# Performance work log

Measured on AMD Instinct MI355X. Metric: run time of the kernel, lower is better.

The kernel has to match this reference:

```python
import jax, jax.numpy as jnp
import numpy as np

N, E = 20000, 100000
D_IN, H1, C1 = 512, 8, 64   # conv1: 512 -> 8 heads x 64, concat -> 512
H2, C2 = 4, 128             # conv2: 512 -> 4 heads x 128, mean -> 128


def setup_inputs() -> dict:
    key = jax.random.key(0)
    k = jax.random.split(key, 12)
    s_in = 1.0 / np.sqrt(D_IN).astype(np.float32)
    return {
        "street_embedding": jax.random.normal(k[0], (N, D_IN), jnp.float32),
        "edge_index": jax.random.randint(k[1], (2, E), 0, N),
        "y": jax.random.randint(k[2], (N,), 0, C2),
        "train_mask": jax.random.bernoulli(k[3], 0.5, (N,)),
        "W1": jax.random.normal(k[4], (D_IN, H1 * C1), jnp.float32) * s_in,
        "att_src1": jax.random.normal(k[5], (H1, C1), jnp.float32) * 0.1,
        "att_dst1": jax.random.normal(k[6], (H1, C1), jnp.float32) * 0.1,
        "b1": jnp.zeros((H1 * C1,), jnp.float32),
        "W2": jax.random.normal(k[7], (H1 * C1, H2 * C2), jnp.float32) * s_in,
        "att_src2": jax.random.normal(k[8], (H2, C2), jnp.float32) * 0.1,
        "att_dst2": jax.random.normal(k[9], (H2, C2), jnp.float32) * 0.1,
        "b2": jnp.zeros((C2,), jnp.float32),
    }


def _gat_conv(x, W, a_src, a_dst, b, src, dst, n, H, C, concat):
    # linear transform (no bias, as in PyG GATConv's internal lin)
    xp = (x @ W).reshape(n, H, C)                      # [N,H,C]
    asrc = jnp.einsum('nhc,hc->nh', xp, a_src)         # [N,H]
    adst = jnp.einsum('nhc,hc->nh', xp, a_dst)
    e = jax.nn.leaky_relu(asrc[src] + adst[dst], 0.2)  # [E',H] edge scores
    # softmax over incoming edges per destination node
    m = jax.lax.stop_gradient(jax.ops.segment_max(e, dst, num_segments=n))
    ex = jnp.exp(e - m[dst])
    denom = jax.ops.segment_sum(ex, dst, num_segments=n)
    alpha = ex / (denom[dst] + 1e-16)                  # [E',H]
    out = jax.ops.segment_sum(alpha[:, :, None] * xp[src], dst, num_segments=n)  # [N,H,C]
    if concat:
        return out.reshape(n, H * C) + b
    return out.mean(axis=1) + b


def reference(street_embedding, edge_index, y, train_mask,
              W1, att_src1, att_dst1, b1, W2, att_src2, att_dst2, b2):
    n = street_embedding.shape[0]
    loop = jnp.arange(n)
    # PyG GATConv adds self-loops by default
    src = jnp.concatenate([edge_index[0], loop])
    dst = jnp.concatenate([edge_index[1], loop])
    # dropout layers are identity in eval mode
    h = _gat_conv(street_embedding, W1, att_src1, att_dst1, b1, src, dst, n, H1, C1, True)
    h = jax.nn.elu(h)
    out = _gat_conv(h, W2, att_src2, att_dst2, b2, src, dst, n, H2, C2, False)  # [N,C2]
    # CrossEntropyLoss, mean over train_mask nodes (weighted mean, jit-safe)
    logp = jax.nn.log_softmax(out, axis=-1)
    ce = -jnp.take_along_axis(logp, y[:, None], axis=-1)[:, 0]
    w = train_mask.astype(out.dtype)
    loss_su = jnp.sum(w * ce) / jnp.sum(w)
    return (loss_su, out)
```

## Files before the change

### kernel.cpp

```cpp
#include <hip/hip_runtime.h>
#include <cmath>

#define D_IN 512
#define HC   512
#define NH1  8
#define NC1  64
#define NH2  4
#define NC2  128
#define BM 128
#define BN 128
#define BK 32

typedef __attribute__((ext_vector_type(8))) short short8;
typedef __attribute__((ext_vector_type(4))) float f32x4;

__device__ inline ushort f2bf(float f) {
  unsigned u = __float_as_uint(f);
  return (ushort)((u + 0x7FFFu + ((u >> 16) & 1u)) >> 16);
}
__device__ inline float bf2f(ushort b) { return __uint_as_float(((unsigned)b) << 16); }

__global__ void k_cast(const float* __restrict__ in, ushort* __restrict__ outp, int n4) {
  int i = blockIdx.x * blockDim.x + threadIdx.x;
  if (i >= n4) return;
  float4 v = ((const float4*)in)[i];
  ushort4 r = { f2bf(v.x), f2bf(v.y), f2bf(v.z), f2bf(v.w) };
  ((ushort4*)outp)[i] = r;
}

__global__ void k_castT(const float* __restrict__ W, ushort* __restrict__ Wt, int K, int N) {
  int idx = blockIdx.x * blockDim.x + threadIdx.x;
  if (idx >= K * N) return;
  int n = idx / K, k = idx - n * K;
  Wt[idx] = f2bf(W[(size_t)k * N + n]);
}

template<int H>
__global__ void k_gemm_bf16(const ushort* __restrict__ A, const ushort* __restrict__ Bt,
                            ushort* __restrict__ Cbf,
                            const float* __restrict__ att_s, const float* __restrict__ att_d,
                            float* __restrict__ asrc, float* __restrict__ adst, int M) {
  constexpr int C = HC / H;
  __shared__ __align__(16) ushort As[BM * BK];
  __shared__ __align__(16) ushort Bs[BN * BK];
  int t = threadIdx.x;
  int m0 = blockIdx.y * BM;
  int n0 = blockIdx.x * BN;
  int wave = t >> 6, lane = t & 63;
  int ln = lane & 15, qd = lane >> 4;
  int wm = (wave >> 1) * 64, wn = (wave & 1) * 64;

  f32x4 acc[4][4] = {};

  int g = t >> 6, ct = (t >> 4) & 3, lt = t & 15;
  int rA0 = m0 + g * 16 + lt;      if (rA0 > M - 1) rA0 = M - 1;
  int rA1 = m0 + 64 + g * 16 + lt; if (rA1 > M - 1) rA1 = M - 1;
  const ushort* gA0 = A + (size_t)rA0 * D_IN + ct * 8;
  const ushort* gA1 = A + (size_t)rA1 * D_IN + ct * 8;
  const ushort* gB0 = Bt + (size_t)(n0 + g * 16 + lt) * D_IN + ct * 8;
  const ushort* gB1 = Bt + (size_t)(n0 + 64 + g * 16 + lt) * D_IN + ct * 8;
  ushort* lA = As + t * 8;
  ushort* lB = Bs + t * 8;

  for (int k0 = 0; k0 < D_IN; k0 += BK) {
    __syncthreads();
    __builtin_amdgcn_global_load_lds((const __attribute__((address_space(1))) void*)(gA0 + k0),
                                     (__attribute__((address_space(3))) void*)lA, 16, 0, 0);
    __builtin_amdgcn_global_load_lds((const __attribute__((address_space(1))) void*)(gA1 + k0),
                                     (__attribute__((address_space(3))) void*)(lA + 2048), 16, 0, 0);
    __builtin_amdgcn_global_load_lds((const __attribute__((address_space(1))) void*)(gB0 + k0),
                                     (__attribute__((address_space(3))) void*)lB, 16, 0, 0);
    __builtin_amdgcn_global_load_lds((const __attribute__((address_space(1))) void*)(gB1 + k0),
                                     (__attribute__((address_space(3))) void*)(lB + 2048), 16, 0, 0);
    __syncthreads();
    short8 a[4], b[4];
#pragma unroll
    for (int i = 0; i < 4; ++i)
      a[i] = *(const short8*)&As[(((wave >> 1) * 4 + i) * 4 + qd) * 128 + ln * 8];
#pragma unroll
    for (int j = 0; j < 4; ++j)
      b[j] = *(const short8*)&Bs[(((wave & 1) * 4 + j) * 4 + qd) * 128 + ln * 8];
#pragma unroll
    for (int i = 0; i < 4; ++i)
#pragma unroll
      for (int j = 0; j < 4; ++j)
        acc[i][j] = __builtin_amdgcn_mfma_f32_16x16x32_bf16(a[i], b[j], acc[i][j], 0, 0, 0);
  }

#pragma unroll
  for (int i = 0; i < 4; ++i) {
#pragma unroll
    for (int reg = 0; reg < 4; ++reg) {
      int row = m0 + wm + i * 16 + qd * 4 + reg;
      if (row >= M) continue;
#pragma unroll
      for (int j = 0; j < 4; ++j)
        Cbf[(size_t)row * HC + n0 + wn + j * 16 + ln] = f2bf(acc[i][j][reg]);
    }
  }

  int colbase = n0 + wn;
  int h = colbase / C;
  float sa[4], da[4];
#pragma unroll
  for (int j = 0; j < 4; ++j) {
    int c = (colbase % C) + j * 16 + ln;
    sa[j] = att_s[h * C + c];
    da[j] = att_d[h * C + c];
  }
#pragma unroll
  for (int i = 0; i < 4; ++i) {
#pragma unroll
    for (int reg = 0; reg < 4; ++reg) {
      float ps = acc[i][0][reg] * sa[0] + acc[i][1][reg] * sa[1]
               + acc[i][2][reg] * sa[2] + acc[i][3][reg] * sa[3];
      float pd = acc[i][0][reg] * da[0] + acc[i][1][reg] * da[1]
               + acc[i][2][reg] * da[2] + acc[i][3][reg] * da[3];
#pragma unroll
      for (int o = 1; o < 16; o <<= 1) { ps += __shfl_xor(ps, o); pd += __shfl_xor(pd, o); }
      int row = m0 + wm + i * 16 + qd * 4 + reg;
      if (ln == 0 && row < M) {
        if (C == 64) { asrc[row * H + h] = ps; adst[row * H + h] = pd; }
        else { atomicAdd(&asrc[row * H + h], ps); atomicAdd(&adst[row * H + h], pd); }
      }
    }
  }
}

__global__ void k_hist(const int* __restrict__ ei, int E, int Etot, int* __restrict__ cnt) {
  int e = blockIdx.x * blockDim.x + threadIdx.x;
  if (e >= Etot) return;
  int d = (e < E) ? ei[E + e] : e - E;
  atomicAdd(&cnt[d], 1);
}

__global__ void k_scan(const int* __restrict__ cnt, int* __restrict__ rowstart, int N) {
  int tid = threadIdx.x;
  int T = (N + 1023) / 1024;
  int base = tid * T;
  int sum = 0;
  for (int i = 0; i < T; ++i) { int j = base + i; if (j < N) sum += cnt[j]; }
  int lane = tid & 63, w = tid >> 6;
  int v = sum;
#pragma unroll
  for (int off = 1; off < 64; off <<= 1) {
    int u = __shfl_up(v, off);
    if (lane >= off) v += u;
  }
  __shared__ int wsum[16];
  if (lane == 63) wsum[w] = v;
  __syncthreads();
  if (tid < 16) {
    int tv = wsum[tid];
#pragma unroll
    for (int off = 1; off < 16; off <<= 1) {
      int u = __shfl_up(tv, off);
      if (tid >= off) tv += u;
    }
    wsum[tid] = tv;
  }
  __syncthreads();
  int wave_prefix = (w == 0) ? 0 : wsum[w - 1];
  int run = wave_prefix + v - sum;
  for (int i = 0; i < T; ++i) {
    int j = base + i;
    if (j < N) { rowstart[j] = run; run += cnt[j]; }
  }
  if (tid == 1023) rowstart[N] = run;
}

__global__ void k_scatter(const int* __restrict__ ei, int E, int Etot,
                          const int* __restrict__ rowstart, int* __restrict__ cursor,
                          int* __restrict__ csr_src) {
  int e = blockIdx.x * blockDim.x + threadIdx.x;
  if (e >= Etot) return;
  int s = (e < E) ? ei[e] : e - E;
  int d = (e < E) ? ei[E + e] : e - E;
  int pos = atomicAdd(&cursor[d], 1);
  csr_src[rowstart[d] + pos] = s;
}

template<int H, int MODE>
__global__ void k_agg(const int* __restrict__ rowstart, const int* __restrict__ csr_src,
                      const float* __restrict__ asrc, const float* __restrict__ adst,
                      const ushort* __restrict__ xp, ushort* __restrict__ hout,
                      float* __restrict__ out2, const float* __restrict__ bias,
                      const int* __restrict__ y, const int* __restrict__ msk,
                      float* __restrict__ acc2, int N) {
  int n = blockIdx.x;
  int tid = threadIdx.x;
  constexpr int C = HC / H;
  int h = (tid * 4) / C;
  int beg = rowstart[n], end = rowstart[n + 1];

  __shared__ int   s_src[32];
  __shared__ float s_out[512];

  float adn = adst[n * H + h];
  float ax = 0.f, ay = 0.f, az = 0.f, aw = 0.f, wsum = 0.f;

  for (int c0 = beg; c0 < end; c0 += 32) {
    int len = end - c0; if (len > 32) len = 32;
    __syncthreads();
    if (tid < len) s_src[tid] = csr_src[c0 + tid];
    __syncthreads();
    for (int i = 0; i < len; ++i) {
      int s = s_src[i];
      float v = asrc[s * H + h] + adn;
      v = (v > 0.f) ? v : 0.2f * v;
      float w = __expf(v);
      ushort4 vv = ((const ushort4*)xp)[(size_t)s * 128 + tid];
      ax += w * bf2f(vv.x); ay += w * bf2f(vv.y);
      az += w * bf2f(vv.z); aw += w * bf2f(vv.w);
      wsum += w;
    }
  }
  float rdn = 1.0f / (wsum + 1e-16f);
  ax *= rdn; ay *= rdn; az *= rdn; aw *= rdn;

  if (MODE == 1) {
    int hc = tid * 4;
    float v0 = ax + bias[hc], v1 = ay + bias[hc + 1];
    float v2 = az + bias[hc + 2], v3 = aw + bias[hc + 3];
    v0 = (v0 > 0.f) ? v0 : expm1f(v0);
    v1 = (v1 > 0.f) ? v1 : expm1f(v1);
    v2 = (v2 > 0.f) ? v2 : expm1f(v2);
    v3 = (v3 > 0.f) ? v3 : expm1f(v3);
    ushort4 rr = { f2bf(v0), f2bf(v1), f2bf(v2), f2bf(v3) };
    ((ushort4*)hout)[(size_t)n * 128 + tid] = rr;
  } else {
    int hc = tid * 4;
    s_out[hc] = ax; s_out[hc + 1] = ay; s_out[hc + 2] = az; s_out[hc + 3] = aw;
    __syncthreads();
    if (tid < 32) {
#pragma unroll
      for (int k = 0; k < 4; ++k) {
        int c = tid * 4 + k;
        float sum = s_out[c] + s_out[128 + c] + s_out[256 + c] + s_out[384 + c];
        float lg = sum * 0.25f + bias[c];
        out2[(size_t)n * NC2 + c] = lg;
        s_out[c] = lg;
      }
    }
    __syncthreads();
    float lv = s_out[tid];
    int lane = tid & 63, wv = tid >> 6;
    float mx = lv;
#pragma unroll
    for (int o = 32; o > 0; o >>= 1) mx = fmaxf(mx, __shfl_xor(mx, o));
    if (lane == 0) s_out[256 + wv] = mx;
    __syncthreads();
    mx = fmaxf(s_out[256], s_out[257]);
    float e = __expf(lv - mx);
#pragma unroll
    for (int o = 32; o > 0; o >>= 1) e += __shfl_xor(e, o);
    if (lane == 0) s_out[260 + wv] = e;
    __syncthreads();
    if (tid == 0 && msk[n] != 0) {
      float se = s_out[260] + s_out[261];
      float ce = mx + logf(se) - s_out[y[n]];
      int slot = n & 127;
      atomicAdd(&acc2[slot], ce);
      atomicAdd(&acc2[128 + slot], 1.0f);
    }
  }
}

__global__ void k_final(const float* __restrict__ acc2, float* __restrict__ out0) {
  int tid = threadIdx.x;
  float ce = acc2[tid], ct = acc2[128 + tid];
#pragma unroll
  for (int o = 32; o > 0; o >>= 1) { ce += __shfl_xor(ce, o); ct += __shfl_xor(ct, o); }
  __shared__ float s[4];
  if ((tid & 63) == 0) { s[(tid >> 6) * 2] = ce; s[(tid >> 6) * 2 + 1] = ct; }
  __syncthreads();
  if (tid == 0) out0[0] = (s[0] + s[2]) / (s[1] + s[3]);
}

extern "C" void kernel_launch(void* const* d_in, const int* in_sizes, int n_in,
                              void* d_out, int out_size, void* d_ws, size_t ws_size,
                              hipStream_t stream) {
  const float* x   = (const float*)d_in[0];
  const int*   ei  = (const int*)d_in[1];
  const int*   y   = (const int*)d_in[2];
  const int*   msk = (const int*)d_in[3];
  const float* W1  = (const float*)d_in[4];
  const float* as1 = (const float*)d_in[5];
  const float* ad1 = (const float*)d_in[6];
  const float* b1  = (const float*)d_in[7];
  const float* W2  = (const float*)d_in[8];
  const float* as2 = (const float*)d_in[9];
  const float* ad2 = (const float*)d_in[10];
  const float* b2  = (const float*)d_in[11];
  float* out = (float*)d_out;

  int N = in_sizes[0] / D_IN;
  int E = in_sizes[1] / 2;
  int Etot = E + N;

  float* ws = (float*)d_ws;
  size_t NF = (size_t)N * HC;
  float* asr1 = ws;
  float* adt1 = asr1 + (size_t)N * NH1;
  float* asr2 = adt1 + (size_t)N * NH1;
  float* adt2 = asr2 + (size_t)N * NH2;
  float* acc2 = adt2 + (size_t)N * NH2;
  int*   cnt    = (int*)(acc2 + 256);
  int*   cursor = cnt + N;
  size_t zero_bytes = ((size_t)N * 2 * NH2 + 256 + 2 * (size_t)N) * sizeof(float);
  int*   rowstart = cursor + N;
  int*   csr_src  = rowstart + N + 1;
  ushort* xpbf = (ushort*)((((uintptr_t)(csr_src + Etot)) + 15) & ~(uintptr_t)15);
  ushort* Abf = xpbf + NF;
  ushort* Wt1 = Abf + NF;
  ushort* Wt2 = Wt1 + (size_t)D_IN * HC;

  hipMemsetAsync(asr2, 0, zero_bytes, stream);

  k_castT<<<(D_IN * HC + 255) / 256, 256, 0, stream>>>(W1, Wt1, D_IN, HC);
  k_castT<<<(D_IN * HC + 255) / 256, 256, 0, stream>>>(W2, Wt2, D_IN, HC);

  k_hist<<<(Etot + 255) / 256, 256, 0, stream>>>(ei, E, Etot, cnt);
  k_scan<<<1, 1024, 0, stream>>>(cnt, rowstart, N);
  k_scatter<<<(Etot + 255) / 256, 256, 0, stream>>>(ei, E, Etot, rowstart, cursor, csr_src);

  dim3 ggrid(HC / BN, (N + BM - 1) / BM);

  k_cast<<<(int)((NF / 4 + 255) / 256), 256, 0, stream>>>(x, Abf, (int)(NF / 4));
  k_gemm_bf16<NH1><<<ggrid, 256, 0, stream>>>(Abf, Wt1, xpbf, as1, ad1, asr1, adt1, N);
  k_agg<NH1, 1><<<N, 128, 0, stream>>>(rowstart, csr_src, asr1, adt1, xpbf, Abf,
                                       nullptr, b1, nullptr, nullptr, nullptr, N);

  k_gemm_bf16<NH2><<<ggrid, 256, 0, stream>>>(Abf, Wt2, xpbf, as2, ad2, asr2, adt2, N);
  k_agg<NH2, 2><<<N, 128, 0, stream>>>(rowstart, csr_src, asr2, adt2, xpbf, nullptr,
                                       out + 1, b2, y, msk, acc2, N);

  k_final<<<1, 128, 0, stream>>>(acc2, out);
}
```

Measured before the change: 299.1 us.

## Double-buffer GEMM LDS tiles, unroll aggregation edge loop, merge weight casts

The bf16 GEMM now keeps two LDS buffers and issues the next K tile's global-to-LDS loads before computing on the current one, removing one barrier per iteration so load latency can overlap with MFMA work. The aggregation kernel processes two edges per iteration so two gathers are in flight at once. The two weight transpose-cast launches are merged into one. LDS use doubles, which may lower GEMM occupancy, and correctness relies on the single barrier per step plus the implicit wait for outstanding LDS-load counters.

```diff
diff --git a/kernel.cpp b/kernel.cpp
--- a/kernel.cpp
+++ b/kernel.cpp
@@ -28,11 +28,16 @@
   ((ushort4*)outp)[i] = r;
 }
 
-__global__ void k_castT(const float* __restrict__ W, ushort* __restrict__ Wt, int K, int N) {
+__global__ void k_castT2(const float* __restrict__ W1, const float* __restrict__ W2,
+                         ushort* __restrict__ Wt1, ushort* __restrict__ Wt2) {
   int idx = blockIdx.x * blockDim.x + threadIdx.x;
-  if (idx >= K * N) return;
-  int n = idx / K, k = idx - n * K;
-  Wt[idx] = f2bf(W[(size_t)k * N + n]);
+  const int KN = D_IN * HC;
+  if (idx >= 2 * KN) return;
+  const float* W = (idx < KN) ? W1 : W2;
+  ushort* Wt = (idx < KN) ? Wt1 : Wt2;
+  int i = (idx < KN) ? idx : idx - KN;
+  int n = i / D_IN, k = i - n * D_IN;
+  Wt[i] = f2bf(W[(size_t)k * HC + n]);
 }
 
 template<int H>
@@ -41,8 +46,8 @@
                             const float* __restrict__ att_s, const float* __restrict__ att_d,
                             float* __restrict__ asrc, float* __restrict__ adst, int M) {
   constexpr int C = HC / H;
-  __shared__ __align__(16) ushort As[BM * BK];
-  __shared__ __align__(16) ushort Bs[BN * BK];
+  __shared__ __align__(16) ushort As[2][BM * BK];
+  __shared__ __align__(16) ushort Bs[2][BN * BK];
   int t = threadIdx.x;
   int m0 = blockIdx.y * BM;
   int n0 = blockIdx.x * BN;
@@ -59,33 +64,43 @@
   const ushort* gA1 = A + (size_t)rA1 * D_IN + ct * 8;
   const ushort* gB0 = Bt + (size_t)(n0 + g * 16 + lt) * D_IN + ct * 8;
   const ushort* gB1 = Bt + (size_t)(n0 + 64 + g * 16 + lt) * D_IN + ct * 8;
-  ushort* lA = As + t * 8;
-  ushort* lB = Bs + t * 8;
-
-  for (int k0 = 0; k0 < D_IN; k0 += BK) {
-    __syncthreads();
-    __builtin_amdgcn_global_load_lds((const __attribute__((address_space(1))) void*)(gA0 + k0),
-                                     (__attribute__((address_space(3))) void*)lA, 16, 0, 0);
-    __builtin_amdgcn_global_load_lds((const __attribute__((address_space(1))) void*)(gA1 + k0),
-                                     (__attribute__((address_space(3))) void*)(lA + 2048), 16, 0, 0);
-    __builtin_amdgcn_global_load_lds((const __attribute__((address_space(1))) void*)(gB0 + k0),
-                                     (__attribute__((address_space(3))) void*)lB, 16, 0, 0);
-    __builtin_amdgcn_global_load_lds((const __attribute__((address_space(1))) void*)(gB1 + k0),
-                                     (__attribute__((address_space(3))) void*)(lB + 2048), 16, 0, 0);
-    __syncthreads();
-    short8 a[4], b[4];
+
+#define ISSUE_TILE(k0, buf)                                                              \
+  do {                                                                                   \
+    __builtin_amdgcn_global_load_lds(                                                    \
+        (const __attribute__((address_space(1))) void*)(gA0 + (k0)),                     \
+        (__attribute__((address_space(3))) void*)(As[buf] + t * 8), 16, 0, 0);           \
+    __builtin_amdgcn_global_load_lds(                                                    \
+        (const __attribute__((address_space(1))) void*)(gA1 + (k0)),                     \
+        (__attribute__((address_space(3))) void*)(As[buf] + 2048 + t * 8), 16, 0, 0);    \
+    __builtin_amdgcn_global_load_lds(                                                    \
+        (const __attribute__((address_space(1))) void*)(gB0 + (k0)),                     \
+        (__attribute__((address_space(3))) void*)(Bs[buf] + t * 8), 16, 0, 0);           \
+    __builtin_amdgcn_global_load_lds(                                                    \
+        (const __attribute__((address_space(1))) void*)(gB1 + (k0)),                     \
+        (__attribute__((address_space(3))) void*)(Bs[buf] + 2048 + t * 8), 16, 0, 0);    \
+  } while (0)
+
+  ISSUE_TILE(0, 0);
+
+  for (int ks = 0; ks < 16; ++ks) {
+    __syncthreads();
+    if (ks < 15) ISSUE_TILE((ks + 1) * BK, (ks + 1) & 1);
+    int b = ks & 1;
+    short8 a[4], bb[4];
 #pragma unroll
     for (int i = 0; i < 4; ++i)
-      a[i] = *(const short8*)&As[(((wave >> 1) * 4 + i) * 4 + qd) * 128 + ln * 8];
+      a[i] = *(const short8*)&As[b][(((wave >> 1) * 4 + i) * 4 + qd) * 128 + ln * 8];
 #pragma unroll
     for (int j = 0; j < 4; ++j)
-      b[j] = *(const short8*)&Bs[(((wave & 1) * 4 + j) * 4 + qd) * 128 + ln * 8];
+      bb[j] = *(const short8*)&Bs[b][(((wave & 1) * 4 + j) * 4 + qd) * 128 + ln * 8];
 #pragma unroll
     for (int i = 0; i < 4; ++i)
 #pragma unroll
       for (int j = 0; j < 4; ++j)
-        acc[i][j] = __builtin_amdgcn_mfma_f32_16x16x32_bf16(a[i], b[j], acc[i][j], 0, 0, 0);
-  }
+        acc[i][j] = __builtin_amdgcn_mfma_f32_16x16x32_bf16(a[i], bb[j], acc[i][j], 0, 0, 0);
+  }
+#undef ISSUE_TILE
 
 #pragma unroll
   for (int i = 0; i < 4; ++i) {
@@ -204,15 +219,31 @@
     __syncthreads();
     if (tid < len) s_src[tid] = csr_src[c0 + tid];
     __syncthreads();
-    for (int i = 0; i < len; ++i) {
-      int s = s_src[i];
-      float v = asrc[s * H + h] + adn;
-      v = (v > 0.f) ? v : 0.2f * v;
-      float w = __expf(v);
-      ushort4 vv = ((const ushort4*)xp)[(size_t)s * 128 + tid];
-      ax += w * bf2f(vv.x); ay += w * bf2f(vv.y);
-      az += w * bf2f(vv.z); aw += w * bf2f(vv.w);
-      wsum += w;
+    int i = 0;
+    for (; i + 1 < len; i += 2) {
+      int s0 = s_src[i], s1 = s_src[i + 1];
+      float v0 = asrc[s0 * H + h] + adn;
+      float v1 = asrc[s1 * H + h] + adn;
+      ushort4 a0 = ((const ushort4*)xp)[(size_t)s0 * 128 + tid];
+      ushort4 a1 = ((const ushort4*)xp)[(size_t)s1 * 128 + tid];
+      v0 = (v0 > 0.f) ? v0 : 0.2f * v0;
+      v1 = (v1 > 0.f) ? v1 : 0.2f * v1;
+      float w0 = __expf(v0), w1 = __expf(v1);
+      ax += w0 * bf2f(a0.x) + w1 * bf2f(a1.x);
+      ay += w0 * bf2f(a0.y) + w1 * bf2f(a1.y);
+      az += w0 * bf2f(a0.z) + w1 * bf2f(a1.z);
+      aw += w0 * bf2f(a0.w) + w1 * bf2f(a1.w);
+      wsum += w0 + w1;
+    }
+    if (i < len) {
+      int s0 = s_src[i];
+      float v0 = asrc[s0 * H + h] + adn;
+      ushort4 a0 = ((const ushort4*)xp)[(size_t)s0 * 128 + tid];
+      v0 = (v0 > 0.f) ? v0 : 0.2f * v0;
+      float w0 = __expf(v0);
+      ax += w0 * bf2f(a0.x); ay += w0 * bf2f(a0.y);
+      az += w0 * bf2f(a0.z); aw += w0 * bf2f(a0.w);
+      wsum += w0;
     }
   }
   float rdn = 1.0f / (wsum + 1e-16f);
@@ -317,8 +348,7 @@
 
   hipMemsetAsync(asr2, 0, zero_bytes, stream);
 
-  k_castT<<<(D_IN * HC + 255) / 256, 256, 0, stream>>>(W1, Wt1, D_IN, HC);
-  k_castT<<<(D_IN * HC + 255) / 256, 256, 0, stream>>>(W2, Wt2, D_IN, HC);
+  k_castT2<<<(2 * D_IN * HC + 255) / 256, 256, 0, stream>>>(W1, W2, Wt1, Wt2);
 
   k_hist<<<(Etot + 255) / 256, 256, 0, stream>>>(ei, E, Etot, cnt);
   k_scan<<<1, 1024, 0, stream>>>(cnt, rowstart, N);
```

Result: no change. 300.2 us (+0.3%).
